# Performance work log

Measured on AMD Instinct MI355X. Metric: run time of the kernel, lower is better.

The kernel has to match this reference:

```python
import jax, jax.numpy as jnp
import numpy as np

NE = 50000   # num edges (nodes of the line graph)
NA = 800000  # adjacency pairs in the edge graph (~avg degree 16)
NC = 100000  # triadic candidates
F = 64       # edge_feat_dim
H = 128      # hidden_dim
L = 3        # num_layers


def setup_inputs() -> dict:
    key = jax.random.key(0)
    ks = iter(jax.random.split(key, 32))

    def w(shape, scale=0.05):
        return jax.random.normal(next(ks), shape, dtype=jnp.float32) * scale

    inp = {
        "edge_features": jax.random.normal(next(ks), (NE, F), dtype=jnp.float32),
        "adj_dst": jnp.sort(jax.random.randint(next(ks), (NA,), 0, NE)),
        "adj_src": jax.random.randint(next(ks), (NA,), 0, NE),
        "cand_i": jax.random.randint(next(ks), (NC,), 0, NE),
        "cand_j": jax.random.randint(next(ks), (NC,), 0, NE),
        # edge encoder: Linear(F,H) -> ReLU -> Linear(H,H)
        "enc_W1": w((F, H)), "enc_b1": jnp.zeros((H,), jnp.float32),
        "enc_W2": w((H, H)), "enc_b2": jnp.zeros((H,), jnp.float32),
        # per-layer message_net: Linear(2H,H) -> ReLU -> Linear(H,H)
        "msg_W1": w((L, 2 * H, H)), "msg_b1": jnp.zeros((L, H), jnp.float32),
        "msg_W2": w((L, H, H)), "msg_b2": jnp.zeros((L, H), jnp.float32),
        # per-layer update_net: Linear(2H,H) -> ReLU -> Linear(H,H)
        "upd_W1": w((L, 2 * H, H)), "upd_b1": jnp.zeros((L, H), jnp.float32),
        "upd_W2": w((L, H, H)), "upd_b2": jnp.zeros((L, H), jnp.float32),
        # triadic predictor: Linear(2H,H)->ReLU->Linear(H,H)->ReLU->Linear(H,1)
        "pred_W1": w((2 * H, H)), "pred_b1": jnp.zeros((H,), jnp.float32),
        "pred_W2": w((H, H)), "pred_b2": jnp.zeros((H,), jnp.float32),
        "pred_W3": w((H, 1)), "pred_b3": jnp.zeros((1,), jnp.float32),
    }
    return inp


def _mlp2(x, W1, b1, W2, b2):
    return jnp.maximum(x @ W1 + b1, 0.0) @ W2 + b2


def reference(edge_features, adj_dst, adj_src, cand_i, cand_j,
              enc_W1, enc_b1, enc_W2, enc_b2,
              msg_W1, msg_b1, msg_W2, msg_b2,
              upd_W1, upd_b1, upd_W2, upd_b2,
              pred_W1, pred_b1, pred_W2, pred_b2, pred_W3, pred_b3):
    # encode edge features -> [NE, H]
    e = _mlp2(edge_features, enc_W1, enc_b1, enc_W2, enc_b2)

    # degree of each edge-node in the line graph
    deg = jax.ops.segment_sum(jnp.ones((adj_dst.shape[0],), e.dtype), adj_dst,
                              num_segments=NE)  # [NE]
    inv_deg = 1.0 / jnp.maximum(deg, 1.0)
    isolated = (deg == 0.0)[:, None]

    for l in range(L):
        # per-pair message: message_net(concat(e_i, e_j))
        pair = jnp.concatenate([e[adj_dst], e[adj_src]], axis=-1)  # [NA, 2H]
        msgs = _mlp2(pair, msg_W1[l], msg_b1[l], msg_W2[l], msg_b2[l])  # [NA, H]
        agg = jax.ops.segment_sum(msgs, adj_dst, num_segments=NE) * inv_deg[:, None]
        # edges with no neighbors: message_net(concat(e_i, e_i))
        self_msg = _mlp2(jnp.concatenate([e, e], axis=-1),
                         msg_W1[l], msg_b1[l], msg_W2[l], msg_b2[l])
        message = jnp.where(isolated, self_msg, agg)
        # update: update_net(concat(e_i, message_i)), then outer ReLU
        e = _mlp2(jnp.concatenate([e, message], axis=-1),
                  upd_W1[l], upd_b1[l], upd_W2[l], upd_b2[l])
        e = jnp.maximum(e, 0.0)

    # triadic predictor on parent-edge pairs (dropout inactive at eval)
    comb = jnp.concatenate([e[cand_i], e[cand_j]], axis=-1)  # [NC, 2H]
    h = jnp.maximum(comb @ pred_W1 + pred_b1, 0.0)
    h = jnp.maximum(h @ pred_W2 + pred_b2, 0.0)
    logits = (h @ pred_W3 + pred_b3)[:, 0]  # [NC]
    probs = jax.nn.sigmoid(logits)
    return probs, logits
```

## Files before the change

### kernel.cpp

```cpp
#include <hip/hip_runtime.h>
#include <hip/hip_bf16.h>

#define NE 50000
#define NA 800000
#define NC 100000

typedef _Float16 f16;
typedef f16 half8 __attribute__((ext_vector_type(8)));
typedef f16 f16x2 __attribute__((ext_vector_type(2)));
typedef float f32x4 __attribute__((ext_vector_type(4)));

#define OFF_ENC1 0
#define OFF_ENC2 8192
#define OFF_MSGPQ 24576
#define OFF_UPD1 122880
#define OFF_UPD2 221184
#define OFF_PREDPQ 270336
#define OFF_PREDW2 303104
#define TOTAL_WT 319488

struct WTArgs {
    const float* src[20];
    int K[20];
    int dstOff[20];
    int dstStride[20];
    int cum[21];
};

__global__ void convert_weights(WTArgs a, f16* __restrict__ wt) {
    int gid = blockIdx.x * 256 + threadIdx.x;
    if (gid >= a.cum[20]) return;
    int j = 0;
#pragma unroll
    for (int i = 1; i < 20; ++i) j += (gid >= a.cum[i]) ? 1 : 0;
    int e = gid - a.cum[j];
    int K = a.K[j];
    int k = e % K;
    int n = e / K;
    wt[a.dstOff[j] + n * a.dstStride[j] + k] = (f16)a.src[j][(size_t)k * 128 + n];
}

__global__ void fuse_w(const float* __restrict__ msg_W2, const float* __restrict__ msg_b2,
                       const float* __restrict__ upd_W1, const float* __restrict__ upd_b1,
                       f16* __restrict__ wt, float* __restrict__ fbias) {
    int gid = blockIdx.x * 256 + threadIdx.x;
    if (gid >= 3 * 128 * 129) return;
    int l = gid / (128 * 129);
    int rem = gid % (128 * 129);
    int n = rem / 129;
    int kk = rem % 129;
    const float* U1b = upd_W1 + (size_t)l * 32768 + 16384;
    if (kk < 128) {
        const float* w2row = msg_W2 + (size_t)l * 16384 + (size_t)kk * 128;
        float s = 0.0f;
        for (int m = 0; m < 128; ++m) s += w2row[m] * U1b[m * 128 + n];
        wt[OFF_UPD1 + l * 32768 + n * 256 + 128 + kk] = (f16)s;
    } else {
        const float* b2 = msg_b2 + l * 128;
        float s = upd_b1[l * 128 + n];
        for (int m = 0; m < 128; ++m) s += b2[m] * U1b[m * 128 + n];
        fbias[l * 128 + n] = s;
    }
}

__global__ void convert_x(const float* __restrict__ x, f16* __restrict__ xb) {
    int i = blockIdx.x * 256 + threadIdx.x;
    if (i < NE * 16) {
        float4 v = ((const float4*)x)[i];
        f16 o0 = (f16)v.x, o1 = (f16)v.y, o2 = (f16)v.z, o3 = (f16)v.w;
        f16x2 a = {o0, o1}, b = {o2, o3};
        ((f16x2*)xb)[i * 2] = a;
        ((f16x2*)xb)[i * 2 + 1] = b;
    }
}

__global__ void deg_kernel(const int* __restrict__ adj_dst, int* __restrict__ degI) {
    int i = blockIdx.x * 256 + threadIdx.x;
    if (i < NA) atomicAdd(&degI[adj_dst[i]], 1);
}

__global__ void seg_kernel(const int* __restrict__ adj_dst, int* __restrict__ segStart) {
    int i = blockIdx.x * 256 + threadIdx.x;
    if (i < NA) {
        int d = adj_dst[i];
        if (i == 0 || adj_dst[i - 1] != d) segStart[d] = i;
    }
}

__global__ __launch_bounds__(256) void pair_agg(
    const f16* __restrict__ P, const f16* __restrict__ Q,
    const int* __restrict__ adj_src, const int* __restrict__ segStart,
    const int* __restrict__ degI, f16* __restrict__ hbar) {
    int w = __builtin_amdgcn_readfirstlane(blockIdx.x * 4 + (threadIdx.x >> 6));
    if (w >= NE) return;
    int lane = threadIdx.x & 63;
    f16x2 p2 = ((const f16x2*)P)[(size_t)w * 64 + lane];
    float p0 = (float)p2.x, p1 = (float)p2.y;
    float a0, a1;
    int deg = degI[w];
    if (deg == 0) {
        f16x2 q2 = ((const f16x2*)Q)[(size_t)w * 64 + lane];
        a0 = fmaxf(p0 + (float)q2.x, 0.0f);
        a1 = fmaxf(p1 + (float)q2.y, 0.0f);
    } else {
        int s = segStart[w];
        float x0 = 0.0f, x1 = 0.0f, y0 = 0.0f, y1 = 0.0f;
        int j = 0;
        for (; j + 1 < deg; j += 2) {
            int sa = adj_src[s + j];
            int sb = adj_src[s + j + 1];
            f16x2 qa = ((const f16x2*)Q)[(size_t)sa * 64 + lane];
            f16x2 qb = ((const f16x2*)Q)[(size_t)sb * 64 + lane];
            x0 += fmaxf(p0 + (float)qa.x, 0.0f);
            x1 += fmaxf(p1 + (float)qa.y, 0.0f);
            y0 += fmaxf(p0 + (float)qb.x, 0.0f);
            y1 += fmaxf(p1 + (float)qb.y, 0.0f);
        }
        if (j < deg) {
            int sa = adj_src[s + j];
            f16x2 qa = ((const f16x2*)Q)[(size_t)sa * 64 + lane];
            x0 += fmaxf(p0 + (float)qa.x, 0.0f);
            x1 += fmaxf(p1 + (float)qa.y, 0.0f);
        }
        float sc = 1.0f / (float)deg;
        a0 = (x0 + y0) * sc;
        a1 = (x1 + y1) * sc;
    }
    f16x2 o;
    o.x = (f16)a0;
    o.y = (f16)a1;
    ((f16x2*)hbar)[(size_t)w * 64 + lane] = o;
}

__global__ __launch_bounds__(512, 2) void pq_kernel(
    const f16* __restrict__ ein, const f16* __restrict__ wpq,
    const float* __restrict__ bP,
    f16* __restrict__ P, f16* __restrict__ Q, int numRows) {
    constexpr int SA = 136;
    __shared__ __align__(16) f16 Abuf[64 * SA];
    const int t = threadIdx.x;
    const int lane = t & 63, wave = t >> 6;
    const int quad = lane >> 4, mn = lane & 15;
    const int sel = wave >> 2;
    const int n0 = (wave & 3) * 32;
    const f16* wt = wpq + (size_t)sel * 128 * 128;
    f16* out = sel ? Q : P;

    half8 wf[4][2];
#pragma unroll
    for (int kc = 0; kc < 4; ++kc)
#pragma unroll
        for (int nt = 0; nt < 2; ++nt)
            wf[kc][nt] = *(const half8*)(wt + (size_t)(n0 + nt * 16 + mn) * 128 + kc * 32 + quad * 8);
    float bc[2];
    bc[0] = sel ? 0.0f : bP[n0 + mn];
    bc[1] = sel ? 0.0f : bP[n0 + 16 + mn];

    const int nTiles = (numRows + 63) >> 6;
    for (int tile = blockIdx.x; tile < nTiles; tile += gridDim.x) {
        const int rbase = tile << 6;
#pragma unroll
        for (int it = 0; it < 2; ++it) {
            int u = it * 512 + t;
            int row = u >> 4;
            int k = (u & 15) * 8;
            int gr = rbase + row;
            half8 v = {};
            if (gr < numRows) v = *(const half8*)(ein + (size_t)gr * 128 + k);
            *(half8*)(Abuf + row * SA + k) = v;
        }
        __syncthreads();
        f32x4 acc[4][2];
#pragma unroll
        for (int mt = 0; mt < 4; ++mt) {
            acc[mt][0] = (f32x4){bc[0], bc[0], bc[0], bc[0]};
            acc[mt][1] = (f32x4){bc[1], bc[1], bc[1], bc[1]};
        }
#pragma unroll
        for (int kc = 0; kc < 4; ++kc) {
            half8 af[4];
#pragma unroll
            for (int mt = 0; mt < 4; ++mt)
                af[mt] = *(const half8*)(Abuf + (mt * 16 + mn) * SA + kc * 32 + quad * 8);
#pragma unroll
            for (int mt = 0; mt < 4; ++mt) {
                acc[mt][0] = __builtin_amdgcn_mfma_f32_16x16x32_f16(af[mt], wf[kc][0], acc[mt][0], 0, 0, 0);
                acc[mt][1] = __builtin_amdgcn_mfma_f32_16x16x32_f16(af[mt], wf[kc][1], acc[mt][1], 0, 0, 0);
            }
        }
#pragma unroll
        for (int mt = 0; mt < 4; ++mt)
#pragma unroll
            for (int nt = 0; nt < 2; ++nt)
#pragma unroll
                for (int r = 0; r < 4; ++r) {
                    int gr = rbase + mt * 16 + quad * 4 + r;
                    if (gr < numRows)
                        out[(size_t)gr * 128 + n0 + nt * 16 + mn] = (f16)acc[mt][nt][r];
                }
        __syncthreads();
    }
}

template <int K1, bool RELU_OUT>
__global__ __launch_bounds__(256, 2) void mlp2_kernel(
    const f16* __restrict__ in0, const f16* __restrict__ in1,
    const f16* __restrict__ w1t, const float* __restrict__ b1,
    const f16* __restrict__ w2t, const float* __restrict__ b2,
    f16* __restrict__ outh, int numRows) {
    constexpr int KC1 = K1 / 32;
    constexpr int SA = K1 + 8;
    constexpr int SH = 136;
    constexpr int ABY = 64 * SA * 2;
    constexpr int HBY = 64 * SH * 2;
    constexpr int BYTES = ABY > HBY ? ABY : HBY;
    __shared__ __align__(16) char U[BYTES];
    f16* Abuf = (f16*)U;
    f16* Hbuf = (f16*)U;

    const int t = threadIdx.x;
    const int lane = t & 63, wave = t >> 6;
    const int quad = lane >> 4, mn = lane & 15;
    const int n0 = wave * 32;

    half8 w1f[KC1][2];
#pragma unroll
    for (int kc = 0; kc < KC1; ++kc)
#pragma unroll
        for (int nt = 0; nt < 2; ++nt)
            w1f[kc][nt] = *(const half8*)(w1t + (size_t)(n0 + nt * 16 + mn) * K1 + kc * 32 + quad * 8);
    half8 w2f[4][2];
#pragma unroll
    for (int kc = 0; kc < 4; ++kc)
#pragma unroll
        for (int nt = 0; nt < 2; ++nt)
            w2f[kc][nt] = *(const half8*)(w2t + (size_t)(n0 + nt * 16 + mn) * 128 + kc * 32 + quad * 8);
    float b1c[2] = {b1[n0 + mn], b1[n0 + 16 + mn]};
    float b2c[2] = {b2[n0 + mn], b2[n0 + 16 + mn]};

    const int nTiles = (numRows + 63) >> 6;
    for (int tile = blockIdx.x; tile < nTiles; tile += gridDim.x) {
        const int rbase = tile << 6;
        constexpr int UPR = K1 / 8;
        constexpr int USH = (K1 == 256) ? 5 : 3;
#pragma unroll
        for (int it = 0; it < (64 * UPR) / 256; ++it) {
            int u = it * 256 + t;
            int row = u >> USH;
            int k = (u & (UPR - 1)) * 8;
            int gr = rbase + row;
            half8 v = {};
            if (gr < numRows) {
                const f16* src;
                if constexpr (K1 == 64)
                    src = in0 + (size_t)gr * 64 + k;
                else
                    src = (k < 128) ? (in0 + (size_t)gr * 128 + k)
                                    : (in1 + (size_t)gr * 128 + (k - 128));
                v = *(const half8*)src;
            }
            *(half8*)(Abuf + row * SA + k) = v;
        }
        __syncthreads();

        f32x4 acc[4][2];
#pragma unroll
        for (int mt = 0; mt < 4; ++mt) {
            acc[mt][0] = (f32x4){b1c[0], b1c[0], b1c[0], b1c[0]};
            acc[mt][1] = (f32x4){b1c[1], b1c[1], b1c[1], b1c[1]};
        }
#pragma unroll
        for (int kc = 0; kc < KC1; ++kc) {
            half8 af[4];
#pragma unroll
            for (int mt = 0; mt < 4; ++mt)
                af[mt] = *(const half8*)(Abuf + (mt * 16 + mn) * SA + kc * 32 + quad * 8);
#pragma unroll
            for (int mt = 0; mt < 4; ++mt) {
                acc[mt][0] = __builtin_amdgcn_mfma_f32_16x16x32_f16(af[mt], w1f[kc][0], acc[mt][0], 0, 0, 0);
                acc[mt][1] = __builtin_amdgcn_mfma_f32_16x16x32_f16(af[mt], w1f[kc][1], acc[mt][1], 0, 0, 0);
            }
        }
        __syncthreads();
#pragma unroll
        for (int mt = 0; mt < 4; ++mt)
#pragma unroll
            for (int nt = 0; nt < 2; ++nt)
#pragma unroll
                for (int r = 0; r < 4; ++r)
                    Hbuf[(mt * 16 + quad * 4 + r) * SH + n0 + nt * 16 + mn] =
                        (f16)fmaxf(acc[mt][nt][r], 0.0f);
        __syncthreads();

        f32x4 acc2[4][2];
#pragma unroll
        for (int mt = 0; mt < 4; ++mt) {
            acc2[mt][0] = (f32x4){b2c[0], b2c[0], b2c[0], b2c[0]};
            acc2[mt][1] = (f32x4){b2c[1], b2c[1], b2c[1], b2c[1]};
        }
#pragma unroll
        for (int kc = 0; kc < 4; ++kc) {
            half8 af[4];
#pragma unroll
            for (int mt = 0; mt < 4; ++mt)
                af[mt] = *(const half8*)(Hbuf + (mt * 16 + mn) * SH + kc * 32 + quad * 8);
#pragma unroll
            for (int mt = 0; mt < 4; ++mt) {
                acc2[mt][0] = __builtin_amdgcn_mfma_f32_16x16x32_f16(af[mt], w2f[kc][0], acc2[mt][0], 0, 0, 0);
                acc2[mt][1] = __builtin_amdgcn_mfma_f32_16x16x32_f16(af[mt], w2f[kc][1], acc2[mt][1], 0, 0, 0);
            }
        }
#pragma unroll
        for (int mt = 0; mt < 4; ++mt)
#pragma unroll
            for (int nt = 0; nt < 2; ++nt)
#pragma unroll
                for (int r = 0; r < 4; ++r) {
                    int gr = rbase + mt * 16 + quad * 4 + r;
                    if (gr < numRows) {
                        float v = acc2[mt][nt][r];
                        if constexpr (RELU_OUT) v = fmaxf(v, 0.0f);
                        outh[(size_t)gr * 128 + n0 + nt * 16 + mn] = (f16)v;
                    }
                }
        __syncthreads();
    }
}

__global__ __launch_bounds__(256, 2) void pred_tail(
    const f16* __restrict__ Pp, const f16* __restrict__ Qp,
    const int* __restrict__ ci, const int* __restrict__ cj,
    const f16* __restrict__ w2t, const float* __restrict__ b2,
    const float* __restrict__ w3, const float* __restrict__ b3,
    float* __restrict__ outProb, float* __restrict__ outLogit, int numRows) {
    constexpr int SA = 136;
    constexpr int SO = 133;
    constexpr int BYTES = (64 * SO * 4 > 64 * SA * 2) ? 64 * SO * 4 : 64 * SA * 2;
    __shared__ __align__(16) char U[BYTES];
    f16* Abuf = (f16*)U;
    float* Obuf = (float*)U;
    __shared__ float w3s[128];
    __shared__ float psum[256];

    const int t = threadIdx.x;
    const int lane = t & 63, wave = t >> 6;
    const int quad = lane >> 4, mn = lane & 15;
    const int n0 = wave * 32;

    if (t < 128) w3s[t] = w3[t];
    float b3v = b3[0];

    half8 wf[4][2];
#pragma unroll
    for (int kc = 0; kc < 4; ++kc)
#pragma unroll
        for (int nt = 0; nt < 2; ++nt)
            wf[kc][nt] = *(const half8*)(w2t + (size_t)(n0 + nt * 16 + mn) * 128 + kc * 32 + quad * 8);
    float b2c[2] = {b2[n0 + mn], b2[n0 + 16 + mn]};

    const int nTiles = (numRows + 63) >> 6;
    for (int tile = blockIdx.x; tile < nTiles; tile += gridDim.x) {
        const int rbase = tile << 6;
#pragma unroll
        for (int it = 0; it < 4; ++it) {
            int u = it * 256 + t;
            int row = u >> 4;
            int k = (u & 15) * 8;
            int gr = rbase + row;
            half8 v = {};
            if (gr < numRows) {
                int i = ci[gr], j = cj[gr];
                half8 a = *(const half8*)(Pp + (size_t)i * 128 + k);
                half8 b = *(const half8*)(Qp + (size_t)j * 128 + k);
#pragma unroll
                for (int x = 0; x < 8; ++x)
                    v[x] = (f16)fmaxf((float)a[x] + (float)b[x], 0.0f);
            }
            *(half8*)(Abuf + row * SA + k) = v;
        }
        __syncthreads();

        f32x4 acc[4][2];
#pragma unroll
        for (int mt = 0; mt < 4; ++mt) {
            acc[mt][0] = (f32x4){b2c[0], b2c[0], b2c[0], b2c[0]};
            acc[mt][1] = (f32x4){b2c[1], b2c[1], b2c[1], b2c[1]};
        }
#pragma unroll
        for (int kc = 0; kc < 4; ++kc) {
            half8 af[4];
#pragma unroll
            for (int mt = 0; mt < 4; ++mt)
                af[mt] = *(const half8*)(Abuf + (mt * 16 + mn) * SA + kc * 32 + quad * 8);
#pragma unroll
            for (int mt = 0; mt < 4; ++mt) {
                acc[mt][0] = __builtin_amdgcn_mfma_f32_16x16x32_f16(af[mt], wf[kc][0], acc[mt][0], 0, 0, 0);
                acc[mt][1] = __builtin_amdgcn_mfma_f32_16x16x32_f16(af[mt], wf[kc][1], acc[mt][1], 0, 0, 0);
            }
        }
        __syncthreads();
#pragma unroll
        for (int mt = 0; mt < 4; ++mt)
#pragma unroll
            for (int nt = 0; nt < 2; ++nt)
#pragma unroll
                for (int r = 0; r < 4; ++r)
                    Obuf[(mt * 16 + quad * 4 + r) * SO + n0 + nt * 16 + mn] =
                        fmaxf(acc[mt][nt][r], 0.0f);
        __syncthreads();
        {
            int row = t & 63, q4 = t >> 6;
            float s = 0.0f;
#pragma unroll
            for (int i = 0; i < 32; ++i)
                s += Obuf[row * SO + q4 * 32 + i] * w3s[q4 * 32 + i];
            psum[t] = s;
        }
        __syncthreads();
        if (t < 64) {
            int gr = rbase + t;
            if (gr < numRows) {
                float lg = psum[t] + psum[t + 64] + psum[t + 128] + psum[t + 192] + b3v;
                outLogit[gr] = lg;
                outProb[gr] = 1.0f / (1.0f + expf(-lg));
            }
        }
        __syncthreads();
    }
}

extern "C" void kernel_launch(void* const* d_in, const int* in_sizes, int n_in,
                              void* d_out, int out_size, void* d_ws, size_t ws_size,
                              hipStream_t stream) {
    const float* edge_features = (const float*)d_in[0];
    const int* adj_dst = (const int*)d_in[1];
    const int* adj_src = (const int*)d_in[2];
    const int* cand_i = (const int*)d_in[3];
    const int* cand_j = (const int*)d_in[4];
    const float* enc_W1 = (const float*)d_in[5];
    const float* enc_b1 = (const float*)d_in[6];
    const float* enc_W2 = (const float*)d_in[7];
    const float* enc_b2 = (const float*)d_in[8];
    const float* msg_W1 = (const float*)d_in[9];
    const float* msg_b1 = (const float*)d_in[10];
    const float* msg_W2 = (const float*)d_in[11];
    const float* msg_b2 = (const float*)d_in[12];
    const float* upd_W1 = (const float*)d_in[13];
    const float* upd_b1 = (const float*)d_in[14];
    const float* upd_W2 = (const float*)d_in[15];
    const float* upd_b2 = (const float*)d_in[16];
    const float* pred_W1 = (const float*)d_in[17];
    const float* pred_b1 = (const float*)d_in[18];
    const float* pred_W2 = (const float*)d_in[19];
    const float* pred_b2 = (const float*)d_in[20];
    const float* pred_W3 = (const float*)d_in[21];
    const float* pred_b3 = (const float*)d_in[22];

    char* ws = (char*)d_ws;
    size_t off = 0;
    auto alloc = [&](size_t bytes) -> void* {
        void* p = ws + off;
        off = (off + bytes + 255) & ~(size_t)255;
        return p;
    };
    f16* wt = (f16*)alloc((size_t)TOTAL_WT * 2);
    float* fbias = (float*)alloc(3 * 128 * 4);
    f16* xb = (f16*)alloc((size_t)NE * 64 * 2);
    f16* eA = (f16*)alloc((size_t)NE * 128 * 2);
    f16* eB = (f16*)alloc((size_t)NE * 128 * 2);
    f16* Pb = (f16*)alloc((size_t)NE * 128 * 2);
    f16* Qb = (f16*)alloc((size_t)NE * 128 * 2);
    f16* hbar = (f16*)alloc((size_t)NE * 128 * 2);
    int* degI = (int*)alloc((size_t)NE * 4);
    int* segStart = (int*)alloc((size_t)NE * 4);

    WTArgs wa;
    int idx = 0, c = 0;
    auto addj = [&](const float* s, int K, int o, int st) {
        wa.src[idx] = s; wa.K[idx] = K; wa.dstOff[idx] = o;
        wa.dstStride[idx] = st; wa.cum[idx] = c;
        c += K * 128; idx++;
    };
    addj(enc_W1, 64, OFF_ENC1, 64);
    addj(enc_W2, 128, OFF_ENC2, 128);
    for (int l = 0; l < 3; ++l) addj(msg_W1 + (size_t)l * 32768, 128, OFF_MSGPQ + l * 32768, 128);
    for (int l = 0; l < 3; ++l) addj(msg_W1 + (size_t)l * 32768 + 16384, 128, OFF_MSGPQ + l * 32768 + 16384, 128);
    for (int l = 0; l < 3; ++l) addj(upd_W1 + (size_t)l * 32768, 128, OFF_UPD1 + l * 32768, 256);
    for (int l = 0; l < 3; ++l) addj(upd_W2 + (size_t)l * 16384, 128, OFF_UPD2 + l * 16384, 128);
    addj(pred_W1, 128, OFF_PREDPQ, 128);
    addj(pred_W1 + 16384, 128, OFF_PREDPQ + 16384, 128);
    addj(pred_W2, 128, OFF_PREDW2, 128);
    for (int i = idx; i <= 20; ++i) wa.cum[i] = c;

    convert_weights<<<(270336 + 255) / 256, 256, 0, stream>>>(wa, wt);
    fuse_w<<<(3 * 128 * 129 + 255) / 256, 256, 0, stream>>>(msg_W2, msg_b2, upd_W1, upd_b1, wt, fbias);
    convert_x<<<(NE * 16 + 255) / 256, 256, 0, stream>>>(edge_features, xb);
    hipMemsetAsync(degI, 0, (size_t)NE * 4, stream);
    deg_kernel<<<(NA + 255) / 256, 256, 0, stream>>>(adj_dst, degI);
    seg_kernel<<<(NA + 255) / 256, 256, 0, stream>>>(adj_dst, segStart);

    const int tilesNE = (NE + 63) / 64;
    mlp2_kernel<64, false><<<tilesNE, 256, 0, stream>>>(
        xb, nullptr, wt + OFF_ENC1, enc_b1, wt + OFF_ENC2, enc_b2, eA, NE);

    f16* cur = eA;
    f16* nxt = eB;
    for (int l = 0; l < 3; ++l) {
        pq_kernel<<<tilesNE, 512, 0, stream>>>(
            cur, wt + OFF_MSGPQ + l * 32768, msg_b1 + l * 128, Pb, Qb, NE);
        pair_agg<<<(NE + 3) / 4, 256, 0, stream>>>(Pb, Qb, adj_src, segStart, degI, hbar);
        mlp2_kernel<256, true><<<tilesNE, 256, 0, stream>>>(
            cur, hbar, wt + OFF_UPD1 + l * 32768, fbias + l * 128,
            wt + OFF_UPD2 + l * 16384, upd_b2 + l * 128, nxt, NE);
        f16* tmp = cur; cur = nxt; nxt = tmp;
    }

    float* outP = (float*)d_out;
    pq_kernel<<<tilesNE, 512, 0, stream>>>(
        cur, wt + OFF_PREDPQ, pred_b1, Pb, Qb, NE);
    pred_tail<<<(NC + 63) / 64, 256, 0, stream>>>(
        Pb, Qb, cand_i, cand_j, wt + OFF_PREDW2, pred_b2, pred_W3, pred_b3,
        outP, outP + NC, NC);

    (void)in_sizes; (void)n_in; (void)out_size; (void)ws_size;
}
```

Before: 439.7 us.

## Fuse P/Q projection into MLP kernels and merge prep/degree kernels

Removes the standalone pq_kernel by computing the next layer's P and Q projections inside the encoder and update MLP kernels, reusing the freshly computed edge tile held in shared memory. This saves re-reading the edge features and several kernel launches. Weight, feature conversion and degree zeroing are merged into one prep kernel, and the degree count and segment-start passes into one kernel. The pair_agg gather loop is unrolled to four neighbors. The fused MLP kernel uses more shared memory and reloads weights per block, which may lower occupancy.

```diff
diff --git a/kernel.cpp b/kernel.cpp
--- a/kernel.cpp
+++ b/kernel.cpp
@@ -27,17 +27,31 @@
     int cum[21];
 };
 
-__global__ void convert_weights(WTArgs a, f16* __restrict__ wt) {
+__global__ void prep_kernel(WTArgs a, const float* __restrict__ x,
+                            f16* __restrict__ wt, f16* __restrict__ xb,
+                            int* __restrict__ degI) {
     int gid = blockIdx.x * 256 + threadIdx.x;
-    if (gid >= a.cum[20]) return;
-    int j = 0;
-#pragma unroll
-    for (int i = 1; i < 20; ++i) j += (gid >= a.cum[i]) ? 1 : 0;
-    int e = gid - a.cum[j];
-    int K = a.K[j];
-    int k = e % K;
-    int n = e / K;
-    wt[a.dstOff[j] + n * a.dstStride[j] + k] = (f16)a.src[j][(size_t)k * 128 + n];
+    if (gid < a.cum[20]) {
+        int j = 0;
+#pragma unroll
+        for (int i = 1; i < 20; ++i) j += (gid >= a.cum[i]) ? 1 : 0;
+        int e = gid - a.cum[j];
+        int K = a.K[j];
+        int k = e % K;
+        int n = e / K;
+        wt[a.dstOff[j] + n * a.dstStride[j] + k] = (f16)a.src[j][(size_t)k * 128 + n];
+        return;
+    }
+    int g2 = gid - a.cum[20];
+    if (g2 < NE * 16) {
+        float4 v = ((const float4*)x)[g2];
+        f16x2 p = {(f16)v.x, (f16)v.y}, q = {(f16)v.z, (f16)v.w};
+        ((f16x2*)xb)[g2 * 2] = p;
+        ((f16x2*)xb)[g2 * 2 + 1] = q;
+        return;
+    }
+    int g3 = g2 - NE * 16;
+    if (g3 < NE) degI[g3] = 0;
 }
 
 __global__ void fuse_w(const float* __restrict__ msg_W2, const float* __restrict__ msg_b2,
@@ -63,26 +77,12 @@
     }
 }
 
-__global__ void convert_x(const float* __restrict__ x, f16* __restrict__ xb) {
-    int i = blockIdx.x * 256 + threadIdx.x;
-    if (i < NE * 16) {
-        float4 v = ((const float4*)x)[i];
-        f16 o0 = (f16)v.x, o1 = (f16)v.y, o2 = (f16)v.z, o3 = (f16)v.w;
-        f16x2 a = {o0, o1}, b = {o2, o3};
-        ((f16x2*)xb)[i * 2] = a;
-        ((f16x2*)xb)[i * 2 + 1] = b;
-    }
-}
-
-__global__ void deg_kernel(const int* __restrict__ adj_dst, int* __restrict__ degI) {
-    int i = blockIdx.x * 256 + threadIdx.x;
-    if (i < NA) atomicAdd(&degI[adj_dst[i]], 1);
-}
-
-__global__ void seg_kernel(const int* __restrict__ adj_dst, int* __restrict__ segStart) {
+__global__ void degseg_kernel(const int* __restrict__ adj_dst, int* __restrict__ degI,
+                              int* __restrict__ segStart) {
     int i = blockIdx.x * 256 + threadIdx.x;
     if (i < NA) {
         int d = adj_dst[i];
+        atomicAdd(&degI[d], 1);
         if (i == 0 || adj_dst[i - 1] != d) segStart[d] = i;
     }
 }
@@ -106,19 +106,25 @@
         int s = segStart[w];
         float x0 = 0.0f, x1 = 0.0f, y0 = 0.0f, y1 = 0.0f;
         int j = 0;
-        for (; j + 1 < deg; j += 2) {
-            int sa = adj_src[s + j];
-            int sb = adj_src[s + j + 1];
-            f16x2 qa = ((const f16x2*)Q)[(size_t)sa * 64 + lane];
-            f16x2 qb = ((const f16x2*)Q)[(size_t)sb * 64 + lane];
+        for (; j + 3 < deg; j += 4) {
+            int s0 = adj_src[s + j], s1 = adj_src[s + j + 1];
+            int s2 = adj_src[s + j + 2], s3 = adj_src[s + j + 3];
+            f16x2 qa = ((const f16x2*)Q)[(size_t)s0 * 64 + lane];
+            f16x2 qb = ((const f16x2*)Q)[(size_t)s1 * 64 + lane];
+            f16x2 qc = ((const f16x2*)Q)[(size_t)s2 * 64 + lane];
+            f16x2 qd = ((const f16x2*)Q)[(size_t)s3 * 64 + lane];
             x0 += fmaxf(p0 + (float)qa.x, 0.0f);
             x1 += fmaxf(p1 + (float)qa.y, 0.0f);
             y0 += fmaxf(p0 + (float)qb.x, 0.0f);
             y1 += fmaxf(p1 + (float)qb.y, 0.0f);
-        }
-        if (j < deg) {
-            int sa = adj_src[s + j];
-            f16x2 qa = ((const f16x2*)Q)[(size_t)sa * 64 + lane];
+            x0 += fmaxf(p0 + (float)qc.x, 0.0f);
+            x1 += fmaxf(p1 + (float)qc.y, 0.0f);
+            y0 += fmaxf(p0 + (float)qd.x, 0.0f);
+            y1 += fmaxf(p1 + (float)qd.y, 0.0f);
+        }
+        for (; j < deg; ++j) {
+            int s0 = adj_src[s + j];
+            f16x2 qa = ((const f16x2*)Q)[(size_t)s0 * 64 + lane];
             x0 += fmaxf(p0 + (float)qa.x, 0.0f);
             x1 += fmaxf(p1 + (float)qa.y, 0.0f);
         }
@@ -132,135 +138,60 @@
     ((f16x2*)hbar)[(size_t)w * 64 + lane] = o;
 }
 
-__global__ __launch_bounds__(512, 2) void pq_kernel(
-    const f16* __restrict__ ein, const f16* __restrict__ wpq,
-    const float* __restrict__ bP,
-    f16* __restrict__ P, f16* __restrict__ Q, int numRows) {
-    constexpr int SA = 136;
-    __shared__ __align__(16) f16 Abuf[64 * SA];
-    const int t = threadIdx.x;
-    const int lane = t & 63, wave = t >> 6;
-    const int quad = lane >> 4, mn = lane & 15;
-    const int sel = wave >> 2;
-    const int n0 = (wave & 3) * 32;
-    const f16* wt = wpq + (size_t)sel * 128 * 128;
-    f16* out = sel ? Q : P;
-
-    half8 wf[4][2];
-#pragma unroll
-    for (int kc = 0; kc < 4; ++kc)
-#pragma unroll
-        for (int nt = 0; nt < 2; ++nt)
-            wf[kc][nt] = *(const half8*)(wt + (size_t)(n0 + nt * 16 + mn) * 128 + kc * 32 + quad * 8);
-    float bc[2];
-    bc[0] = sel ? 0.0f : bP[n0 + mn];
-    bc[1] = sel ? 0.0f : bP[n0 + 16 + mn];
-
-    const int nTiles = (numRows + 63) >> 6;
-    for (int tile = blockIdx.x; tile < nTiles; tile += gridDim.x) {
-        const int rbase = tile << 6;
-#pragma unroll
-        for (int it = 0; it < 2; ++it) {
-            int u = it * 512 + t;
-            int row = u >> 4;
-            int k = (u & 15) * 8;
-            int gr = rbase + row;
-            half8 v = {};
-            if (gr < numRows) v = *(const half8*)(ein + (size_t)gr * 128 + k);
-            *(half8*)(Abuf + row * SA + k) = v;
-        }
-        __syncthreads();
-        f32x4 acc[4][2];
-#pragma unroll
-        for (int mt = 0; mt < 4; ++mt) {
-            acc[mt][0] = (f32x4){bc[0], bc[0], bc[0], bc[0]};
-            acc[mt][1] = (f32x4){bc[1], bc[1], bc[1], bc[1]};
-        }
-#pragma unroll
-        for (int kc = 0; kc < 4; ++kc) {
-            half8 af[4];
-#pragma unroll
-            for (int mt = 0; mt < 4; ++mt)
-                af[mt] = *(const half8*)(Abuf + (mt * 16 + mn) * SA + kc * 32 + quad * 8);
-#pragma unroll
-            for (int mt = 0; mt < 4; ++mt) {
-                acc[mt][0] = __builtin_amdgcn_mfma_f32_16x16x32_f16(af[mt], wf[kc][0], acc[mt][0], 0, 0, 0);
-                acc[mt][1] = __builtin_amdgcn_mfma_f32_16x16x32_f16(af[mt], wf[kc][1], acc[mt][1], 0, 0, 0);
-            }
-        }
-#pragma unroll
-        for (int mt = 0; mt < 4; ++mt)
-#pragma unroll
-            for (int nt = 0; nt < 2; ++nt)
-#pragma unroll
-                for (int r = 0; r < 4; ++r) {
-                    int gr = rbase + mt * 16 + quad * 4 + r;
-                    if (gr < numRows)
-                        out[(size_t)gr * 128 + n0 + nt * 16 + mn] = (f16)acc[mt][nt][r];
-                }
-        __syncthreads();
-    }
-}
-
 template <int K1, bool RELU_OUT>
-__global__ __launch_bounds__(256, 2) void mlp2_kernel(
+__global__ __launch_bounds__(256, 2) void mlp2pq_kernel(
     const f16* __restrict__ in0, const f16* __restrict__ in1,
     const f16* __restrict__ w1t, const float* __restrict__ b1,
     const f16* __restrict__ w2t, const float* __restrict__ b2,
-    f16* __restrict__ outh, int numRows) {
+    f16* __restrict__ oute,
+    const f16* __restrict__ wpq, const float* __restrict__ bP,
+    f16* __restrict__ P, f16* __restrict__ Q, int numRows) {
     constexpr int KC1 = K1 / 32;
     constexpr int SA = K1 + 8;
     constexpr int SH = 136;
     constexpr int ABY = 64 * SA * 2;
-    constexpr int HBY = 64 * SH * 2;
-    constexpr int BYTES = ABY > HBY ? ABY : HBY;
+    constexpr int HEBY = 64 * SH * 2 * 2;
+    constexpr int BYTES = ABY > HEBY ? ABY : HEBY;
     __shared__ __align__(16) char U[BYTES];
     f16* Abuf = (f16*)U;
     f16* Hbuf = (f16*)U;
+    f16* Ebuf = (f16*)(U + 64 * SH * 2);
 
     const int t = threadIdx.x;
     const int lane = t & 63, wave = t >> 6;
     const int quad = lane >> 4, mn = lane & 15;
     const int n0 = wave * 32;
-
-    half8 w1f[KC1][2];
-#pragma unroll
-    for (int kc = 0; kc < KC1; ++kc)
-#pragma unroll
-        for (int nt = 0; nt < 2; ++nt)
-            w1f[kc][nt] = *(const half8*)(w1t + (size_t)(n0 + nt * 16 + mn) * K1 + kc * 32 + quad * 8);
-    half8 w2f[4][2];
-#pragma unroll
-    for (int kc = 0; kc < 4; ++kc)
-#pragma unroll
-        for (int nt = 0; nt < 2; ++nt)
-            w2f[kc][nt] = *(const half8*)(w2t + (size_t)(n0 + nt * 16 + mn) * 128 + kc * 32 + quad * 8);
-    float b1c[2] = {b1[n0 + mn], b1[n0 + 16 + mn]};
-    float b2c[2] = {b2[n0 + mn], b2[n0 + 16 + mn]};
-
-    const int nTiles = (numRows + 63) >> 6;
-    for (int tile = blockIdx.x; tile < nTiles; tile += gridDim.x) {
-        const int rbase = tile << 6;
-        constexpr int UPR = K1 / 8;
-        constexpr int USH = (K1 == 256) ? 5 : 3;
-#pragma unroll
-        for (int it = 0; it < (64 * UPR) / 256; ++it) {
-            int u = it * 256 + t;
-            int row = u >> USH;
-            int k = (u & (UPR - 1)) * 8;
-            int gr = rbase + row;
-            half8 v = {};
-            if (gr < numRows) {
-                const f16* src;
-                if constexpr (K1 == 64)
-                    src = in0 + (size_t)gr * 64 + k;
-                else
-                    src = (k < 128) ? (in0 + (size_t)gr * 128 + k)
-                                    : (in1 + (size_t)gr * 128 + (k - 128));
-                v = *(const half8*)src;
-            }
-            *(half8*)(Abuf + row * SA + k) = v;
-        }
+    const int rbase = blockIdx.x << 6;
+
+    constexpr int UPR = K1 / 8;
+    constexpr int USH = (K1 == 256) ? 5 : 3;
+#pragma unroll
+    for (int it = 0; it < (64 * UPR) / 256; ++it) {
+        int u = it * 256 + t;
+        int row = u >> USH;
+        int k = (u & (UPR - 1)) * 8;
+        int gr = rbase + row;
+        half8 v = {};
+        if (gr < numRows) {
+            const f16* src;
+            if constexpr (K1 == 64)
+                src = in0 + (size_t)gr * 64 + k;
+            else
+                src = (k < 128) ? (in0 + (size_t)gr * 128 + k)
+                                : (in1 + (size_t)gr * 128 + (k - 128));
+            v = *(const half8*)src;
+        }
+        *(half8*)(Abuf + row * SA + k) = v;
+    }
+
+    {
+        half8 w1f[KC1][2];
+#pragma unroll
+        for (int kc = 0; kc < KC1; ++kc)
+#pragma unroll
+            for (int nt = 0; nt < 2; ++nt)
+                w1f[kc][nt] = *(const half8*)(w1t + (size_t)(n0 + nt * 16 + mn) * K1 + kc * 32 + quad * 8);
+        float b1c[2] = {b1[n0 + mn], b1[n0 + 16 + mn]};
         __syncthreads();
 
         f32x4 acc[4][2];
@@ -291,6 +222,16 @@
                     Hbuf[(mt * 16 + quad * 4 + r) * SH + n0 + nt * 16 + mn] =
                         (f16)fmaxf(acc[mt][nt][r], 0.0f);
         __syncthreads();
+    }
+
+    {
+        half8 w2f[4][2];
+#pragma unroll
+        for (int kc = 0; kc < 4; ++kc)
+#pragma unroll
+            for (int nt = 0; nt < 2; ++nt)
+                w2f[kc][nt] = *(const half8*)(w2t + (size_t)(n0 + nt * 16 + mn) * 128 + kc * 32 + quad * 8);
+        float b2c[2] = {b2[n0 + mn], b2[n0 + 16 + mn]};
 
         f32x4 acc2[4][2];
 #pragma unroll
@@ -316,14 +257,90 @@
             for (int nt = 0; nt < 2; ++nt)
 #pragma unroll
                 for (int r = 0; r < 4; ++r) {
+                    float v = acc2[mt][nt][r];
+                    if constexpr (RELU_OUT) v = fmaxf(v, 0.0f);
+                    f16 hv = (f16)v;
+                    int lr = mt * 16 + quad * 4 + r;
+                    Ebuf[lr * SH + n0 + nt * 16 + mn] = hv;
+                    int gr = rbase + lr;
+                    if (gr < numRows) oute[(size_t)gr * 128 + n0 + nt * 16 + mn] = hv;
+                }
+        __syncthreads();
+    }
+
+    {
+        half8 wpa[4][2];
+#pragma unroll
+        for (int kc = 0; kc < 4; ++kc)
+#pragma unroll
+            for (int nt = 0; nt < 2; ++nt)
+                wpa[kc][nt] = *(const half8*)(wpq + (size_t)(n0 + nt * 16 + mn) * 128 + kc * 32 + quad * 8);
+        float bpc[2] = {bP[n0 + mn], bP[n0 + 16 + mn]};
+        f32x4 accp[4][2];
+#pragma unroll
+        for (int mt = 0; mt < 4; ++mt) {
+            accp[mt][0] = (f32x4){bpc[0], bpc[0], bpc[0], bpc[0]};
+            accp[mt][1] = (f32x4){bpc[1], bpc[1], bpc[1], bpc[1]};
+        }
+#pragma unroll
+        for (int kc = 0; kc < 4; ++kc) {
+            half8 af[4];
+#pragma unroll
+            for (int mt = 0; mt < 4; ++mt)
+                af[mt] = *(const half8*)(Ebuf + (mt * 16 + mn) * SH + kc * 32 + quad * 8);
+#pragma unroll
+            for (int mt = 0; mt < 4; ++mt) {
+                accp[mt][0] = __builtin_amdgcn_mfma_f32_16x16x32_f16(af[mt], wpa[kc][0], accp[mt][0], 0, 0, 0);
+                accp[mt][1] = __builtin_amdgcn_mfma_f32_16x16x32_f16(af[mt], wpa[kc][1], accp[mt][1], 0, 0, 0);
+            }
+        }
+#pragma unroll
+        for (int mt = 0; mt < 4; ++mt)
+#pragma unroll
+            for (int nt = 0; nt < 2; ++nt)
+#pragma unroll
+                for (int r = 0; r < 4; ++r) {
                     int gr = rbase + mt * 16 + quad * 4 + r;
-                    if (gr < numRows) {
-                        float v = acc2[mt][nt][r];
-                        if constexpr (RELU_OUT) v = fmaxf(v, 0.0f);
-                        outh[(size_t)gr * 128 + n0 + nt * 16 + mn] = (f16)v;
-                    }
+                    if (gr < numRows)
+                        P[(size_t)gr * 128 + n0 + nt * 16 + mn] = (f16)accp[mt][nt][r];
                 }
-        __syncthreads();
+    }
+
+    {
+        half8 wpb[4][2];
+#pragma unroll
+        for (int kc = 0; kc < 4; ++kc)
+#pragma unroll
+            for (int nt = 0; nt < 2; ++nt)
+                wpb[kc][nt] = *(const half8*)(wpq + 16384 + (size_t)(n0 + nt * 16 + mn) * 128 + kc * 32 + quad * 8);
+        f32x4 accq[4][2];
+#pragma unroll
+        for (int mt = 0; mt < 4; ++mt) {
+            accq[mt][0] = (f32x4){0.0f, 0.0f, 0.0f, 0.0f};
+            accq[mt][1] = (f32x4){0.0f, 0.0f, 0.0f, 0.0f};
+        }
+#pragma unroll
+        for (int kc = 0; kc < 4; ++kc) {
+            half8 af[4];
+#pragma unroll
+            for (int mt = 0; mt < 4; ++mt)
+                af[mt] = *(const half8*)(Ebuf + (mt * 16 + mn) * SH + kc * 32 + quad * 8);
+#pragma unroll
+            for (int mt = 0; mt < 4; ++mt) {
+                accq[mt][0] = __builtin_amdgcn_mfma_f32_16x16x32_f16(af[mt], wpb[kc][0], accq[mt][0], 0, 0, 0);
+                accq[mt][1] = __builtin_amdgcn_mfma_f32_16x16x32_f16(af[mt], wpb[kc][1], accq[mt][1], 0, 0, 0);
+            }
+        }
+#pragma unroll
+        for (int mt = 0; mt < 4; ++mt)
+#pragma unroll
+            for (int nt = 0; nt < 2; ++nt)
+#pragma unroll
+                for (int r = 0; r < 4; ++r) {
+                    int gr = rbase + mt * 16 + quad * 4 + r;
+                    if (gr < numRows)
+                        Q[(size_t)gr * 128 + n0 + nt * 16 + mn] = (f16)accq[mt][nt][r];
+                }
     }
 }
 
@@ -492,32 +509,31 @@
     addj(pred_W2, 128, OFF_PREDW2, 128);
     for (int i = idx; i <= 20; ++i) wa.cum[i] = c;
 
-    convert_weights<<<(270336 + 255) / 256, 256, 0, stream>>>(wa, wt);
+    const int prepN = 270336 + NE * 16 + NE;
+    prep_kernel<<<(prepN + 255) / 256, 256, 0, stream>>>(wa, edge_features, wt, xb, degI);
     fuse_w<<<(3 * 128 * 129 + 255) / 256, 256, 0, stream>>>(msg_W2, msg_b2, upd_W1, upd_b1, wt, fbias);
-    convert_x<<<(NE * 16 + 255) / 256, 256, 0, stream>>>(edge_features, xb);
-    hipMemsetAsync(degI, 0, (size_t)NE * 4, stream);
-    deg_kernel<<<(NA + 255) / 256, 256, 0, stream>>>(adj_dst, degI);
-    seg_kernel<<<(NA + 255) / 256, 256, 0, stream>>>(adj_dst, segStart);
+    degseg_kernel<<<(NA + 255) / 256, 256, 0, stream>>>(adj_dst, degI, segStart);
 
     const int tilesNE = (NE + 63) / 64;
-    mlp2_kernel<64, false><<<tilesNE, 256, 0, stream>>>(
-        xb, nullptr, wt + OFF_ENC1, enc_b1, wt + OFF_ENC2, enc_b2, eA, NE);
+
+    mlp2pq_kernel<64, false><<<tilesNE, 256, 0, stream>>>(
+        xb, nullptr, wt + OFF_ENC1, enc_b1, wt + OFF_ENC2, enc_b2, eA,
+        wt + OFF_MSGPQ, msg_b1, Pb, Qb, NE);
 
     f16* cur = eA;
     f16* nxt = eB;
     for (int l = 0; l < 3; ++l) {
-        pq_kernel<<<tilesNE, 512, 0, stream>>>(
-            cur, wt + OFF_MSGPQ + l * 32768, msg_b1 + l * 128, Pb, Qb, NE);
         pair_agg<<<(NE + 3) / 4, 256, 0, stream>>>(Pb, Qb, adj_src, segStart, degI, hbar);
-        mlp2_kernel<256, true><<<tilesNE, 256, 0, stream>>>(
+        const f16* wpq = (l < 2) ? (wt + OFF_MSGPQ + (l + 1) * 32768) : (wt + OFF_PREDPQ);
+        const float* bP = (l < 2) ? (msg_b1 + (l + 1) * 128) : pred_b1;
+        mlp2pq_kernel<256, true><<<tilesNE, 256, 0, stream>>>(
             cur, hbar, wt + OFF_UPD1 + l * 32768, fbias + l * 128,
-            wt + OFF_UPD2 + l * 16384, upd_b2 + l * 128, nxt, NE);
+            wt + OFF_UPD2 + l * 16384, upd_b2 + l * 128, nxt,
+            wpq, bP, Pb, Qb, NE);
         f16* tmp = cur; cur = nxt; nxt = tmp;
     }
 
     float* outP = (float*)d_out;
-    pq_kernel<<<tilesNE, 512, 0, stream>>>(
-        cur, wt + OFF_PREDPQ, pred_b1, Pb, Qb, NE);
     pred_tail<<<(NC + 63) / 64, 256, 0, stream>>>(
         Pb, Qb, cand_i, cand_j, wt + OFF_PREDW2, pred_b2, pred_W3, pred_b3,
         outP, outP + NC, NC);
```

New measurement: 392.9 us. -10.6%, faster.
